# Optimization experiments

Hardware: AMD Instinct MI355X
Metric: run time of the kernel (lower is better)

## Reference

```python
import jax, jax.numpy as jnp
import numpy as np

B, T, C, H = 8, 2048, 768, 64  # batch, seq, n_embed, head_size

def setup_inputs() -> dict:
    key = jax.random.key(0)
    kx, kq, kk, kv = jax.random.split(key, 4)
    x = jax.random.normal(kx, (B, T, C), dtype=jnp.float32)
    Wq = jax.random.normal(kq, (C, H), dtype=jnp.float32) * (C ** -0.5)
    Wk = jax.random.normal(kk, (C, H), dtype=jnp.float32) * (C ** -0.5)
    Wv = jax.random.normal(kv, (C, H), dtype=jnp.float32) * (C ** -0.5)
    return {"x": x, "Wq": Wq, "Wk": Wk, "Wv": Wv}

def reference(x, Wq, Wk, Wv):
    # projections (bias-free linears)
    q = jnp.einsum('btc,ch->bth', x, Wq)
    k = jnp.einsum('btc,ch->bth', x, Wk)
    v = jnp.einsum('btc,ch->bth', x, Wv)
    scale = k.shape[-1] ** -0.5
    wei = jnp.einsum('bth,bsh->bts', q, k) * scale  # [B, T, T]
    Tq = x.shape[1]
    causal = jnp.tril(jnp.ones((Tq, Tq), dtype=bool))
    wei = jnp.where(causal, wei, -jnp.inf)
    wei = jax.nn.softmax(wei, axis=-1)
    # dropout p=0.0 -> identity
    out = jnp.einsum('bts,bsh->bth', wei, v)
    return out
```

## Files before the change

kernel.cpp:

```cpp
#include <hip/hip_runtime.h>


typedef __bf16 bf16x8 __attribute__((ext_vector_type(8)));
typedef float  f32x4  __attribute__((ext_vector_type(4)));
typedef unsigned int u32;

union ABu {
    bf16x8 v;
    uint4  u;
    unsigned short us[8];
};

__device__ __forceinline__ unsigned short f2bf(float f) {
    union { float f; unsigned int u; } c; c.f = f;
    unsigned int u = c.u + 0x7fffu + ((c.u >> 16) & 1u);
    return (unsigned short)(u >> 16);
}

__device__ __forceinline__ void gld16(void* lds, const void* g) {
    __builtin_amdgcn_global_load_lds(
        (const u32 __attribute__((address_space(1)))*)g,
        (u32 __attribute__((address_space(3)))*)lds, 16, 0, 0);
}

__global__ __launch_bounds__(256)
void wt_kernel(const float* __restrict__ Wq, const float* __restrict__ Wk,
               const float* __restrict__ Wv, unsigned short* __restrict__ wF) {
    const int j   = blockIdx.x / 6;
    const int kgg = blockIdx.x % 6;
    const int t = threadIdx.x;
    const int kg = kgg * 4 + (t >> 6);
    const int lane = t & 63, quad = lane >> 4, l16 = lane & 15;
    const int m = j >> 2, nb = (j & 3) * 16;
    const float* W = (m == 0) ? Wq : (m == 1) ? Wk : Wv;
    ABu o;
#pragma unroll
    for (int i = 0; i < 8; ++i)
        o.us[i] = f2bf(W[(kg * 32 + quad * 8 + i) * 64 + nb + l16]);
    *(uint4*)(wF + ((size_t)(j * 24 + kg) * 64 + lane) * 8) = o.u;
}

__global__ __launch_bounds__(512, 4)
void qkv_kernel(const float* __restrict__ x, const unsigned short* __restrict__ wF,
                unsigned short* __restrict__ qF, unsigned short* __restrict__ kF,
                unsigned short* __restrict__ vF) {
    __shared__ float          xs[32][68];
    __shared__ unsigned short wsW[24][64][8];
    __shared__ unsigned short Cst[2][12][16][17];
    const int tid  = threadIdx.x;
    const int lane = tid & 63, w = tid >> 6;
    const int l16  = lane & 15, quad = lane >> 4;
    const int mh   = w & 1, nh = w >> 1;
    const int m0   = blockIdx.x * 32;
    const int b    = m0 >> 11;

    f32x4 acc[3];
#pragma unroll
    for (int j = 0; j < 3; ++j) acc[j] = (f32x4){0.f, 0.f, 0.f, 0.f};

    const int xrow = tid >> 4, xc16 = tid & 15;

    for (int kk = 0; kk < 12; ++kk) {
        __syncthreads();
#pragma unroll
        for (int i = 0; i < 3; ++i) {
            const int c = w * 3 + i;
            const int j = c >> 1, kg2 = c & 1;
            gld16((char*)wsW + (size_t)c * 1024 + lane * 16,
                  (const char*)wF + ((size_t)(j * 24 + kk * 2 + kg2) * 64 + lane) * 16);
        }
        *(float4*)&xs[xrow][xc16 * 4] =
            *(const float4*)&x[(size_t)(m0 + xrow) * 768 + kk * 64 + xc16 * 4];
        __syncthreads();

#pragma unroll
        for (int kg2 = 0; kg2 < 2; ++kg2) {
            const float* xr = &xs[mh * 16 + l16][kg2 * 32 + quad * 8];
            float4 f0 = *(const float4*)xr;
            float4 f1 = *(const float4*)(xr + 4);
            ABu af;
            af.us[0] = f2bf(f0.x); af.us[1] = f2bf(f0.y);
            af.us[2] = f2bf(f0.z); af.us[3] = f2bf(f0.w);
            af.us[4] = f2bf(f1.x); af.us[5] = f2bf(f1.y);
            af.us[6] = f2bf(f1.z); af.us[7] = f2bf(f1.w);
#pragma unroll
            for (int jl = 0; jl < 3; ++jl) {
                const int j = nh * 3 + jl;
                ABu bf;
                bf.u = *(const uint4*)((char*)wsW + (size_t)(j * 2 + kg2) * 1024 + lane * 16);
                acc[jl] = __builtin_amdgcn_mfma_f32_16x16x32_bf16(af.v, bf.v, acc[jl], 0, 0, 0);
            }
        }
    }

    __syncthreads();
#pragma unroll
    for (int jl = 0; jl < 3; ++jl)
#pragma unroll
        for (int r = 0; r < 4; ++r)
            Cst[mh][nh * 3 + jl][quad * 4 + r][l16] = f2bf(acc[jl][r]);
    __syncthreads();

    const int g = tid >> 6, el = tid & 63;
    const int eq = el >> 4, e16 = el & 15;
    if (g < 4) {
        const int mhh = g >> 1, kg = g & 1;
        ABu oq, ok;
#pragma unroll
        for (int i = 0; i < 8; ++i) {
            const int h = kg * 32 + eq * 8 + i;
            oq.us[i] = Cst[mhh][h >> 4][e16][h & 15];
            ok.us[i] = Cst[mhh][4 + (h >> 4)][e16][h & 15];
        }
        const size_t tt = (size_t)b * 128 + ((m0 & 2047) >> 4) + mhh;
        *(uint4*)(qF + ((tt * 2 + kg) * 64 + el) * 8) = oq.u;
        *(uint4*)(kF + ((tt * 2 + kg) * 64 + el) * 8) = ok.u;
    } else {
        const int nt = g & 3;
        const int sv = (m0 & 2047) >> 6, kg = (m0 >> 5) & 1;
        ABu ov;
#pragma unroll
        for (int i = 0; i < 8; ++i) {
            const int loc = eq * 8 + i;
            ov.us[i] = Cst[loc >> 4][8 + nt][loc & 15][e16];
        }
        *(uint4*)(vF + ((((size_t)(b * 32 + sv) * 4 + nt) * 2 + kg) * 64 + el) * 8) = ov.u;
    }
}

__global__ __launch_bounds__(256, 4)
void attn_kernel(const unsigned short* __restrict__ qF,
                 const unsigned short* __restrict__ kF,
                 const unsigned short* __restrict__ vF,
                 float* __restrict__ opart, float* __restrict__ lpart) {
    __shared__ unsigned short PT[4][64][20];
    const int tid  = threadIdx.x;
    const int lane = tid & 63, w = tid >> 6;
    const int l16  = lane & 15, quad = lane >> 4;
    const int idx  = blockIdx.x;
    const int b    = idx >> 7;
    const int rem  = idx & 127;
    const int jj   = rem >> 2, quarter = rem & 3;
    const int qs   = (jj & 1) ? (31 - (jj >> 1)) : (jj >> 1);
    const int tt   = qs * 4 + w;
    const int tq0  = tt * 16;
    const float L2E = 1.44269504089f;
    const float MFIX = 16.0f;

    ABu aq[2];
#pragma unroll
    for (int kg = 0; kg < 2; ++kg)
        aq[kg].u = *(const uint4*)(qF + ((((size_t)b * 128 + tt) * 2 + kg) * 64 + lane) * 8);

    f32x4 acc[4];
#pragma unroll
    for (int nt = 0; nt < 4; ++nt) acc[nt] = (f32x4){0.f, 0.f, 0.f, 0.f};
    float lrow[4] = {0.f, 0.f, 0.f, 0.f};

    for (int st = quarter; st <= qs; st += 4) {
        const int s0 = st * 64;
        const unsigned short* kbase = kF + (size_t)(b * 128 + st * 4) * 2 * 512;
        const unsigned short* vbase = vF + (size_t)(b * 32 + st) * 8 * 512;
        ABu kf[8];
#pragma unroll
        for (int c = 0; c < 8; ++c)
            kf[c].u = *(const uint4*)(kbase + (size_t)c * 512 + lane * 8);
        float p[4][4];
#pragma unroll
        for (int nt = 0; nt < 4; ++nt) {
            f32x4 s = (f32x4){0.f, 0.f, 0.f, 0.f};
            s = __builtin_amdgcn_mfma_f32_16x16x32_bf16(aq[0].v, kf[nt * 2 + 0].v, s, 0, 0, 0);
            s = __builtin_amdgcn_mfma_f32_16x16x32_bf16(aq[1].v, kf[nt * 2 + 1].v, s, 0, 0, 0);
            const int sg = s0 + nt * 16 + l16;
#pragma unroll
            for (int r = 0; r < 4; ++r) {
                float sc = (sg > tq0 + quad * 4 + r) ? -1e30f : s[r] * 0.125f;
                float pv = exp2f((sc - MFIX) * L2E);
                p[nt][r] = pv;
                lrow[r] += pv;
            }
        }
        ABu vf[8];
#pragma unroll
        for (int c = 0; c < 8; ++c)
            vf[c].u = *(const uint4*)(vbase + (size_t)c * 512 + lane * 8);
#pragma unroll
        for (int nt = 0; nt < 4; ++nt) {
            ushort4 pw;
            pw.x = f2bf(p[nt][0]); pw.y = f2bf(p[nt][1]);
            pw.z = f2bf(p[nt][2]); pw.w = f2bf(p[nt][3]);
            *(ushort4*)&PT[w][nt * 16 + l16][quad * 4] = pw;
        }
        ABu ap[2];
#pragma unroll
        for (int ks = 0; ks < 2; ++ks)
#pragma unroll
            for (int j = 0; j < 8; ++j)
                ap[ks].us[j] = PT[w][ks * 32 + quad * 8 + j][l16];
#pragma unroll
        for (int nt = 0; nt < 4; ++nt) {
            acc[nt] = __builtin_amdgcn_mfma_f32_16x16x32_bf16(ap[0].v, vf[nt * 2 + 0].v, acc[nt], 0, 0, 0);
            acc[nt] = __builtin_amdgcn_mfma_f32_16x16x32_bf16(ap[1].v, vf[nt * 2 + 1].v, acc[nt], 0, 0, 0);
        }
    }

#pragma unroll
    for (int off = 1; off <= 8; off <<= 1)
#pragma unroll
        for (int r = 0; r < 4; ++r)
            lrow[r] += __shfl_xor(lrow[r], off);

    float* obase = opart + ((size_t)(quarter * 8 + b) * 2048 + tq0) * 64;
#pragma unroll
    for (int nt = 0; nt < 4; ++nt)
#pragma unroll
        for (int r = 0; r < 4; ++r)
            obase[(size_t)(quad * 4 + r) * 64 + nt * 16 + l16] = acc[nt][r];
    if (l16 == 0) {
#pragma unroll
        for (int r = 0; r < 4; ++r)
            lpart[(size_t)(quarter * 8 + b) * 2048 + tq0 + quad * 4 + r] = lrow[r];
    }
}

__global__ __launch_bounds__(256)
void finalize_kernel(const float* __restrict__ opart, const float* __restrict__ lpart,
                     float* __restrict__ out) {
    const int idx = blockIdx.x * 256 + threadIdx.x;
    const int row = idx >> 4;
    float4 v = ((const float4*)opart)[idx];
    float  l = lpart[row];
#pragma unroll
    for (int q = 1; q < 4; ++q) {
        float4 u = ((const float4*)opart)[(size_t)q * 262144 + idx];
        v.x += u.x; v.y += u.y; v.z += u.z; v.w += u.w;
        l += lpart[(size_t)q * 16384 + row];
    }
    const float li = 1.f / l;
    v.x *= li; v.y *= li; v.z *= li; v.w *= li;
    ((float4*)out)[idx] = v;
}

extern "C" void kernel_launch(void* const* d_in, const int* in_sizes, int n_in,
                              void* d_out, int out_size, void* d_ws, size_t ws_size,
                              hipStream_t stream) {
    const float* x  = (const float*)d_in[0];
    const float* Wq = (const float*)d_in[1];
    const float* Wk = (const float*)d_in[2];
    const float* Wv = (const float*)d_in[3];
    float* out = (float*)d_out;

    char* ws = (char*)d_ws;
    unsigned short* wF    = (unsigned short*)ws;
    unsigned short* qF    = (unsigned short*)(ws + (512 << 10));
    unsigned short* kF    = (unsigned short*)(ws + (512 << 10) + (2 << 20));
    unsigned short* vF    = (unsigned short*)(ws + (512 << 10) + (4 << 20));
    float*          opart = (float*)(ws + (512 << 10) + (6 << 20));
    float*          lpart = (float*)(ws + (512 << 10) + (22 << 20));

    wt_kernel<<<72, 256, 0, stream>>>(Wq, Wk, Wv, wF);
    qkv_kernel<<<512, 512, 0, stream>>>(x, wF, qF, kF, vF);
    attn_kernel<<<1024, 256, 0, stream>>>(qF, kF, vF, opart, lpart);
    finalize_kernel<<<1024, 256, 0, stream>>>(opart, lpart, out);
}
```

Measured before the change: 132.4 us.

## Stage K/V tiles in double-buffered LDS shared across eight waves per block

```diff
diff --git a/kernel.cpp b/kernel.cpp
--- a/kernel.cpp
+++ b/kernel.cpp
@@ -128,22 +128,25 @@
     }
 }
 
-__global__ __launch_bounds__(256, 4)
+__global__ __launch_bounds__(512, 4)
 void attn_kernel(const unsigned short* __restrict__ qF,
                  const unsigned short* __restrict__ kF,
                  const unsigned short* __restrict__ vF,
                  float* __restrict__ opart, float* __restrict__ lpart) {
-    __shared__ unsigned short PT[4][64][20];
+    __shared__ unsigned short KS[2][8][64][8];
+    __shared__ unsigned short VS[2][8][64][8];
+    __shared__ unsigned short PT[8][64][20];
     const int tid  = threadIdx.x;
     const int lane = tid & 63, w = tid >> 6;
     const int l16  = lane & 15, quad = lane >> 4;
     const int idx  = blockIdx.x;
-    const int b    = idx >> 7;
-    const int rem  = idx & 127;
+    const int b    = idx >> 6;
+    const int rem  = idx & 63;
     const int jj   = rem >> 2, quarter = rem & 3;
-    const int qs   = (jj & 1) ? (31 - (jj >> 1)) : (jj >> 1);
-    const int tt   = qs * 4 + w;
+    const int qsuper = (jj & 1) ? (15 - (jj >> 1)) : (jj >> 1);
+    const int tt   = qsuper * 8 + w;
     const int tq0  = tt * 16;
+    const int stmax = 2 * qsuper + 1;
     const float L2E = 1.44269504089f;
     const float MFIX = 16.0f;
 
@@ -157,51 +160,69 @@
     for (int nt = 0; nt < 4; ++nt) acc[nt] = (f32x4){0.f, 0.f, 0.f, 0.f};
     float lrow[4] = {0.f, 0.f, 0.f, 0.f};
 
-    for (int st = quarter; st <= qs; st += 4) {
+    const size_t stgoff = (size_t)w * 1024 + lane * 16;
+
+    if (quarter <= stmax) {
+        const char* ksrc = (const char*)(kF + (size_t)(b * 128 + quarter * 4) * 1024);
+        const char* vsrc = (const char*)(vF + (size_t)(b * 32 + quarter) * 4096);
+        gld16((char*)KS + stgoff, ksrc + stgoff);
+        gld16((char*)VS + stgoff, vsrc + stgoff);
+    }
+    __syncthreads();
+
+    int cur = 0;
+    for (int st = quarter; st <= stmax; st += 4) {
+        const int nxt = st + 4;
+        if (nxt <= stmax) {
+            const char* ksrc = (const char*)(kF + (size_t)(b * 128 + nxt * 4) * 1024);
+            const char* vsrc = (const char*)(vF + (size_t)(b * 32 + nxt) * 4096);
+            gld16((char*)KS + (size_t)(cur ^ 1) * 8192 + stgoff, ksrc + stgoff);
+            gld16((char*)VS + (size_t)(cur ^ 1) * 8192 + stgoff, vsrc + stgoff);
+        }
         const int s0 = st * 64;
-        const unsigned short* kbase = kF + (size_t)(b * 128 + st * 4) * 2 * 512;
-        const unsigned short* vbase = vF + (size_t)(b * 32 + st) * 8 * 512;
-        ABu kf[8];
-#pragma unroll
-        for (int c = 0; c < 8; ++c)
-            kf[c].u = *(const uint4*)(kbase + (size_t)c * 512 + lane * 8);
-        float p[4][4];
-#pragma unroll
-        for (int nt = 0; nt < 4; ++nt) {
-            f32x4 s = (f32x4){0.f, 0.f, 0.f, 0.f};
-            s = __builtin_amdgcn_mfma_f32_16x16x32_bf16(aq[0].v, kf[nt * 2 + 0].v, s, 0, 0, 0);
-            s = __builtin_amdgcn_mfma_f32_16x16x32_bf16(aq[1].v, kf[nt * 2 + 1].v, s, 0, 0, 0);
-            const int sg = s0 + nt * 16 + l16;
-#pragma unroll
-            for (int r = 0; r < 4; ++r) {
-                float sc = (sg > tq0 + quad * 4 + r) ? -1e30f : s[r] * 0.125f;
-                float pv = exp2f((sc - MFIX) * L2E);
-                p[nt][r] = pv;
-                lrow[r] += pv;
-            }
-        }
-        ABu vf[8];
-#pragma unroll
-        for (int c = 0; c < 8; ++c)
-            vf[c].u = *(const uint4*)(vbase + (size_t)c * 512 + lane * 8);
-#pragma unroll
-        for (int nt = 0; nt < 4; ++nt) {
-            ushort4 pw;
-            pw.x = f2bf(p[nt][0]); pw.y = f2bf(p[nt][1]);
-            pw.z = f2bf(p[nt][2]); pw.w = f2bf(p[nt][3]);
-            *(ushort4*)&PT[w][nt * 16 + l16][quad * 4] = pw;
-        }
-        ABu ap[2];
-#pragma unroll
-        for (int ks = 0; ks < 2; ++ks)
-#pragma unroll
-            for (int j = 0; j < 8; ++j)
-                ap[ks].us[j] = PT[w][ks * 32 + quad * 8 + j][l16];
-#pragma unroll
-        for (int nt = 0; nt < 4; ++nt) {
-            acc[nt] = __builtin_amdgcn_mfma_f32_16x16x32_bf16(ap[0].v, vf[nt * 2 + 0].v, acc[nt], 0, 0, 0);
-            acc[nt] = __builtin_amdgcn_mfma_f32_16x16x32_bf16(ap[1].v, vf[nt * 2 + 1].v, acc[nt], 0, 0, 0);
-        }
+        if (s0 <= tq0 + 15) {
+            float p[4][4];
+#pragma unroll
+            for (int nt = 0; nt < 4; ++nt) {
+                ABu k0, k1;
+                k0.u = *(const uint4*)((char*)KS + (size_t)cur * 8192 + (nt * 2 + 0) * 1024 + lane * 16);
+                k1.u = *(const uint4*)((char*)KS + (size_t)cur * 8192 + (nt * 2 + 1) * 1024 + lane * 16);
+                f32x4 s = (f32x4){0.f, 0.f, 0.f, 0.f};
+                s = __builtin_amdgcn_mfma_f32_16x16x32_bf16(aq[0].v, k0.v, s, 0, 0, 0);
+                s = __builtin_amdgcn_mfma_f32_16x16x32_bf16(aq[1].v, k1.v, s, 0, 0, 0);
+                const int sg = s0 + nt * 16 + l16;
+#pragma unroll
+                for (int r = 0; r < 4; ++r) {
+                    float sc = (sg > tq0 + quad * 4 + r) ? -1e30f : s[r] * 0.125f;
+                    float pv = exp2f((sc - MFIX) * L2E);
+                    p[nt][r] = pv;
+                    lrow[r] += pv;
+                }
+            }
+#pragma unroll
+            for (int nt = 0; nt < 4; ++nt) {
+                ushort4 pw;
+                pw.x = f2bf(p[nt][0]); pw.y = f2bf(p[nt][1]);
+                pw.z = f2bf(p[nt][2]); pw.w = f2bf(p[nt][3]);
+                *(ushort4*)&PT[w][nt * 16 + l16][quad * 4] = pw;
+            }
+            ABu ap[2];
+#pragma unroll
+            for (int ks = 0; ks < 2; ++ks)
+#pragma unroll
+                for (int j = 0; j < 8; ++j)
+                    ap[ks].us[j] = PT[w][ks * 32 + quad * 8 + j][l16];
+#pragma unroll
+            for (int nt = 0; nt < 4; ++nt) {
+                ABu v0, v1;
+                v0.u = *(const uint4*)((char*)VS + (size_t)cur * 8192 + (nt * 2 + 0) * 1024 + lane * 16);
+                v1.u = *(const uint4*)((char*)VS + (size_t)cur * 8192 + (nt * 2 + 1) * 1024 + lane * 16);
+                acc[nt] = __builtin_amdgcn_mfma_f32_16x16x32_bf16(ap[0].v, v0.v, acc[nt], 0, 0, 0);
+                acc[nt] = __builtin_amdgcn_mfma_f32_16x16x32_bf16(ap[1].v, v1.v, acc[nt], 0, 0, 0);
+            }
+        }
+        __syncthreads();
+        cur ^= 1;
     }
 
 #pragma unroll
@@ -260,6 +281,6 @@
 
     wt_kernel<<<72, 256, 0, stream>>>(Wq, Wk, Wv, wF);
     qkv_kernel<<<512, 512, 0, stream>>>(x, wF, qF, kF, vF);
-    attn_kernel<<<1024, 256, 0, stream>>>(qF, kF, vF, opart, lpart);
+    attn_kernel<<<512, 512, 0, stream>>>(qF, kF, vF, opart, lpart);
     finalize_kernel<<<1024, 256, 0, stream>>>(opart, lpart, out);
 }
```

Result: no change. 132.8 us (+0.3%).

## Double-buffer QKV projection loads and store attention partials in bf16

Applied to the files above, without the earlier changes.

```diff
diff --git a/kernel.cpp b/kernel.cpp
--- a/kernel.cpp
+++ b/kernel.cpp
@@ -15,6 +15,10 @@
     union { float f; unsigned int u; } c; c.f = f;
     unsigned int u = c.u + 0x7fffu + ((c.u >> 16) & 1u);
     return (unsigned short)(u >> 16);
+}
+__device__ __forceinline__ float bf2f(unsigned short s) {
+    union { unsigned int u; float f; } c; c.u = ((unsigned int)s) << 16;
+    return c.f;
 }
 
 __device__ __forceinline__ void gld16(void* lds, const void* g) {
@@ -44,8 +48,8 @@
 void qkv_kernel(const float* __restrict__ x, const unsigned short* __restrict__ wF,
                 unsigned short* __restrict__ qF, unsigned short* __restrict__ kF,
                 unsigned short* __restrict__ vF) {
-    __shared__ float          xs[32][68];
-    __shared__ unsigned short wsW[24][64][8];
+    __shared__ float          xs[2][32][68];
+    __shared__ unsigned short wsW[2][24][64][8];
     __shared__ unsigned short Cst[2][12][16][17];
     const int tid  = threadIdx.x;
     const int lane = tid & 63, w = tid >> 6;
@@ -60,22 +64,32 @@
 
     const int xrow = tid >> 4, xc16 = tid & 15;
 
+#pragma unroll
+    for (int i = 0; i < 3; ++i) {
+        const int c = w * 3 + i, j = c >> 1, kg2 = c & 1;
+        gld16((char*)wsW[0] + (size_t)c * 1024 + lane * 16,
+              (const char*)wF + ((size_t)(j * 24 + kg2) * 64 + lane) * 16);
+    }
+    *(float4*)&xs[0][xrow][xc16 * 4] =
+        *(const float4*)&x[(size_t)(m0 + xrow) * 768 + xc16 * 4];
+    __syncthreads();
+
     for (int kk = 0; kk < 12; ++kk) {
-        __syncthreads();
-#pragma unroll
-        for (int i = 0; i < 3; ++i) {
-            const int c = w * 3 + i;
-            const int j = c >> 1, kg2 = c & 1;
-            gld16((char*)wsW + (size_t)c * 1024 + lane * 16,
-                  (const char*)wF + ((size_t)(j * 24 + kk * 2 + kg2) * 64 + lane) * 16);
-        }
-        *(float4*)&xs[xrow][xc16 * 4] =
-            *(const float4*)&x[(size_t)(m0 + xrow) * 768 + kk * 64 + xc16 * 4];
-        __syncthreads();
+        const int cur = kk & 1, nxt = cur ^ 1;
+        float4 xn;
+        if (kk + 1 < 12) {
+#pragma unroll
+            for (int i = 0; i < 3; ++i) {
+                const int c = w * 3 + i, j = c >> 1, kg2 = c & 1;
+                gld16((char*)wsW[nxt] + (size_t)c * 1024 + lane * 16,
+                      (const char*)wF + ((size_t)(j * 24 + (kk + 1) * 2 + kg2) * 64 + lane) * 16);
+            }
+            xn = *(const float4*)&x[(size_t)(m0 + xrow) * 768 + (kk + 1) * 64 + xc16 * 4];
+        }
 
 #pragma unroll
         for (int kg2 = 0; kg2 < 2; ++kg2) {
-            const float* xr = &xs[mh * 16 + l16][kg2 * 32 + quad * 8];
+            const float* xr = &xs[cur][mh * 16 + l16][kg2 * 32 + quad * 8];
             float4 f0 = *(const float4*)xr;
             float4 f1 = *(const float4*)(xr + 4);
             ABu af;
@@ -87,13 +101,16 @@
             for (int jl = 0; jl < 3; ++jl) {
                 const int j = nh * 3 + jl;
                 ABu bf;
-                bf.u = *(const uint4*)((char*)wsW + (size_t)(j * 2 + kg2) * 1024 + lane * 16);
+                bf.u = *(const uint4*)((char*)wsW[cur] + (size_t)(j * 2 + kg2) * 1024 + lane * 16);
                 acc[jl] = __builtin_amdgcn_mfma_f32_16x16x32_bf16(af.v, bf.v, acc[jl], 0, 0, 0);
             }
         }
-    }
-
-    __syncthreads();
+
+        if (kk + 1 < 12)
+            *(float4*)&xs[nxt][xrow][xc16 * 4] = xn;
+        __syncthreads();
+    }
+
 #pragma unroll
     for (int jl = 0; jl < 3; ++jl)
 #pragma unroll
@@ -132,7 +149,7 @@
 void attn_kernel(const unsigned short* __restrict__ qF,
                  const unsigned short* __restrict__ kF,
                  const unsigned short* __restrict__ vF,
-                 float* __restrict__ opart, float* __restrict__ lpart) {
+                 unsigned short* __restrict__ opart, float* __restrict__ lpart) {
     __shared__ unsigned short PT[4][64][20];
     const int tid  = threadIdx.x;
     const int lane = tid & 63, w = tid >> 6;
@@ -159,8 +176,8 @@
 
     for (int st = quarter; st <= qs; st += 4) {
         const int s0 = st * 64;
-        const unsigned short* kbase = kF + (size_t)(b * 128 + st * 4) * 2 * 512;
-        const unsigned short* vbase = vF + (size_t)(b * 32 + st) * 8 * 512;
+        const unsigned short* kbase = kF + (size_t)(b * 128 + st * 4) * 1024;
+        const unsigned short* vbase = vF + (size_t)(b * 32 + st) * 4096;
         ABu kf[8];
 #pragma unroll
         for (int c = 0; c < 8; ++c)
@@ -210,12 +227,12 @@
         for (int r = 0; r < 4; ++r)
             lrow[r] += __shfl_xor(lrow[r], off);
 
-    float* obase = opart + ((size_t)(quarter * 8 + b) * 2048 + tq0) * 64;
+    unsigned short* obase = opart + ((size_t)(quarter * 8 + b) * 2048 + tq0) * 64;
 #pragma unroll
     for (int nt = 0; nt < 4; ++nt)
 #pragma unroll
         for (int r = 0; r < 4; ++r)
-            obase[(size_t)(quad * 4 + r) * 64 + nt * 16 + l16] = acc[nt][r];
+            obase[(size_t)(quad * 4 + r) * 64 + nt * 16 + l16] = f2bf(acc[nt][r]);
     if (l16 == 0) {
 #pragma unroll
         for (int r = 0; r < 4; ++r)
@@ -224,16 +241,16 @@
 }
 
 __global__ __launch_bounds__(256)
-void finalize_kernel(const float* __restrict__ opart, const float* __restrict__ lpart,
-                     float* __restrict__ out) {
+void finalize_kernel(const unsigned short* __restrict__ opart,
+                     const float* __restrict__ lpart, float* __restrict__ out) {
     const int idx = blockIdx.x * 256 + threadIdx.x;
     const int row = idx >> 4;
-    float4 v = ((const float4*)opart)[idx];
-    float  l = lpart[row];
-#pragma unroll
-    for (int q = 1; q < 4; ++q) {
-        float4 u = ((const float4*)opart)[(size_t)q * 262144 + idx];
-        v.x += u.x; v.y += u.y; v.z += u.z; v.w += u.w;
+    float4 v = (float4){0.f, 0.f, 0.f, 0.f};
+    float  l = 0.f;
+#pragma unroll
+    for (int q = 0; q < 4; ++q) {
+        ushort4 u = ((const ushort4*)opart)[(size_t)q * 262144 + idx];
+        v.x += bf2f(u.x); v.y += bf2f(u.y); v.z += bf2f(u.z); v.w += bf2f(u.w);
         l += lpart[(size_t)q * 16384 + row];
     }
     const float li = 1.f / l;
@@ -255,8 +272,8 @@
     unsigned short* qF    = (unsigned short*)(ws + (512 << 10));
     unsigned short* kF    = (unsigned short*)(ws + (512 << 10) + (2 << 20));
     unsigned short* vF    = (unsigned short*)(ws + (512 << 10) + (4 << 20));
-    float*          opart = (float*)(ws + (512 << 10) + (6 << 20));
-    float*          lpart = (float*)(ws + (512 << 10) + (22 << 20));
+    unsigned short* opart = (unsigned short*)(ws + (512 << 10) + (6 << 20));
+    float*          lpart = (float*)(ws + (512 << 10) + (14 << 20));
 
     wt_kernel<<<72, 256, 0, stream>>>(Wq, Wk, Wv, wF);
     qkv_kernel<<<512, 512, 0, stream>>>(x, wF, qF, kF, vF);
```

After: 128.1 us. 3.3% less time.
